# Kernel optimization log

Hardware: AMD Instinct MI355X
Metric: run time of the kernel (lower is better)

Reference implementation:

```python
import jax, jax.numpy as jnp
import numpy as np

KW, KH = 8, 8   # kernel_size = (kw, kh) per torch module indexing
SW, SH = 4, 4   # stride_size = (sw, sh)


def setup_inputs() -> dict:
    key = jax.random.key(0)
    x = jax.random.normal(key, (4, 128, 128, 128), dtype=jnp.float32)  # [B, C, H, W]
    return {"x": x}


def _local_autocorr(x, kh=KH, kw=KW, sh=SH, sw=SW):
    B, C, H, W = x.shape
    nh = (H - kh) // sh + 1
    nw = (W - kw) // sw + 1
    # Background is x zero-padded by (kh//2, (kh+1)//2 - 1) vertically and
    # (kw//2, (kw+1)//2 - 1) horizontally -> background patches are (2kh-1, 2kw-1).
    xp = jnp.pad(x, ((0, 0), (0, 0),
                     (kh // 2, (kh + 1) // 2 - 1),
                     (kw // 2, (kw + 1) // 2 - 1)))

    # For each shift (dy, dx) in [0,kh)x[0,kw):
    #   ret[b,iy,ix,c,dy,dx] = sum_{u,v} x[b,c,top+u,left+v] * xp[b,c,top+dy+u,left+dx+v]
    # i.e. elementwise product with the shifted map, then sum-pool with window (kh,kw), stride (sh,sw).
    def step(carry, s):
        dy = s // kw
        dx = s % kw
        shifted = jax.lax.dynamic_slice(xp, (0, 0, dy, dx), (B, C, H, W))
        prod = x * shifted
        pooled = jax.lax.reduce_window(prod, 0.0, jax.lax.add,
                                       (1, 1, kh, kw), (1, 1, sh, sw), 'VALID')
        return carry, pooled  # [B, C, nh, nw]

    _, stacked = jax.lax.scan(step, None, jnp.arange(kh * kw))
    # stacked: [kh*kw, B, C, nh, nw] with shift index s = dy*kw + dx
    out = stacked.reshape(kh, kw, B, C, nh, nw)
    out = jnp.transpose(out, (2, 4, 5, 3, 0, 1))  # [B, nh, nw, C, kh, kw]
    return out


def reference(x):
    return _local_autocorr(x)
```

## Files before the change

kernel.cpp:

```cpp
#include <hip/hip_runtime.h>


#define Bn 4
#define Cn 128
#define Hn 128
#define Wn 128
#define NH 31
#define NW 31
#define CB 16
#define PXT 4
#define PYT 4
#define TROWS 27
#define RST 28
#define CST (TROWS*RST)
#define F4C (TROWS*7)
#define PST 273

__global__ __launch_bounds__(256, 3)
void lac_kernel(const float* __restrict__ x, float* __restrict__ out) {
    __shared__ float sm[CB * CST];

    const int bid = blockIdx.x;
    const int ct = bid & 7;
    const int tx = (bid >> 3) & 7;
    const int ty = (bid >> 6) & 7;
    const int b  = bid >> 9;
    const int c0 = ct * CB;
    const int gy0 = ty * (PYT * 4) - 4;
    const int gx0 = tx * (PXT * 4) - 4;
    const int tid = threadIdx.x;

    for (int i = tid; i < CB * F4C; i += 256) {
        const int c   = i / F4C;
        const int rem = i - c * F4C;
        const int r   = rem / 7;
        const int q   = rem - r * 7;
        const int y   = gy0 + r;
        const int xc  = gx0 + q * 4;
        const float* src = x + (((size_t)(b * Cn + c0 + c) * Hn + y) * Wn + xc);
        float4 v;
        if (y >= 0 && y < Hn && xc >= 0 && xc + 3 < Wn) {
            v = *reinterpret_cast<const float4*>(src);
        } else if (y >= 0 && y < Hn) {
            v.x = (xc + 0 >= 0 && xc + 0 < Wn) ? src[0] : 0.0f;
            v.y = (xc + 1 >= 0 && xc + 1 < Wn) ? src[1] : 0.0f;
            v.z = (xc + 2 >= 0 && xc + 2 < Wn) ? src[2] : 0.0f;
            v.w = (xc + 3 >= 0 && xc + 3 < Wn) ? src[3] : 0.0f;
        } else {
            v = make_float4(0.0f, 0.0f, 0.0f, 0.0f);
        }
        reinterpret_cast<float4*>(sm)[i] = v;
    }
    __syncthreads();

    const int cs  = tid & 15;
    const int pos = tid >> 4;
    const int px  = pos & 3;
    const int py  = pos >> 2;
    const float* rg = &sm[cs * CST + (py * 4) * RST + px * 4];

    float acc[8][8];
#pragma unroll
    for (int i = 0; i < 8; ++i)
#pragma unroll
        for (int j = 0; j < 8; ++j) acc[i][j] = 0.0f;

#pragma unroll
    for (int r = 0; r < 15; ++r) {
        float rw[16];
        float4 q0 = *reinterpret_cast<const float4*>(&rg[r * RST + 0]);
        float4 q1 = *reinterpret_cast<const float4*>(&rg[r * RST + 4]);
        float4 q2 = *reinterpret_cast<const float4*>(&rg[r * RST + 8]);
        float4 q3 = *reinterpret_cast<const float4*>(&rg[r * RST + 12]);
        rw[0]  = q0.x; rw[1]  = q0.y; rw[2]  = q0.z; rw[3]  = q0.w;
        rw[4]  = q1.x; rw[5]  = q1.y; rw[6]  = q1.z; rw[7]  = q1.w;
        rw[8]  = q2.x; rw[9]  = q2.y; rw[10] = q2.z; rw[11] = q2.w;
        rw[12] = q3.x; rw[13] = q3.y; rw[14] = q3.z; rw[15] = q3.w;
#pragma unroll
        for (int u = 0; u < 8; ++u) {
            const int dy = r - u;
            if (dy >= 0 && dy < 8) {
                float4 b0 = *reinterpret_cast<const float4*>(&rg[(u + 4) * RST + 4]);
                float4 b1 = *reinterpret_cast<const float4*>(&rg[(u + 4) * RST + 8]);
                float bsr[8];
                bsr[0] = b0.x; bsr[1] = b0.y; bsr[2] = b0.z; bsr[3] = b0.w;
                bsr[4] = b1.x; bsr[5] = b1.y; bsr[6] = b1.z; bsr[7] = b1.w;
#pragma unroll
                for (int v = 0; v < 8; ++v) {
                    const float bv = bsr[v];
#pragma unroll
                    for (int dx = 0; dx < 8; ++dx)
                        acc[dy][dx] = fmaf(bv, rw[v + dx], acc[dy][dx]);
                }
            }
        }
    }

    float4* lds4 = reinterpret_cast<float4*>(sm);
#pragma unroll
    for (int rnd = 0; rnd < 2; ++rnd) {
        __syncthreads();
        if ((pos >> 3) == rnd) {
            const int p = pos & 7;
#pragma unroll
            for (int dy = 0; dy < 8; ++dy) {
                lds4[p * PST + cs * 17 + dy * 2 + 0] =
                    make_float4(acc[dy][0], acc[dy][1], acc[dy][2], acc[dy][3]);
                lds4[p * PST + cs * 17 + dy * 2 + 1] =
                    make_float4(acc[dy][4], acc[dy][5], acc[dy][6], acc[dy][7]);
            }
        }
        __syncthreads();
#pragma unroll
        for (int p = 0; p < 8; ++p) {
            const int pp  = rnd * 8 + p;
            const int ppx = pp & 3;
            const int ppy = pp >> 2;
            const int iy  = ty * PYT + ppy;
            const int ix  = tx * PXT + ppx;
            if (iy < NH && ix < NW) {
                float4* obase = reinterpret_cast<float4*>(
                    out + ((((size_t)b * NH + iy) * NW + ix) * Cn + c0) * 64);
                const int c   = tid >> 4;
                const int rem = tid & 15;
                obase[tid] = lds4[p * PST + c * 17 + rem];
            }
        }
    }
}

extern "C" void kernel_launch(void* const* d_in, const int* in_sizes, int n_in,
                              void* d_out, int out_size, void* d_ws, size_t ws_size,
                              hipStream_t stream) {
    const float* x = (const float*)d_in[0];
    float* out = (float*)d_out;
    lac_kernel<<<dim3(2048), dim3(256), 0, stream>>>(x, out);
}
```

Before: 94.35 us.

## Retile blocks to 8 channels by 8x4 positions and rework output staging

```diff
diff --git a/kernel.cpp b/kernel.cpp
--- a/kernel.cpp
+++ b/kernel.cpp
@@ -7,22 +7,24 @@
 #define Wn 128
 #define NH 31
 #define NW 31
-#define CB 16
-#define PXT 4
+#define CB 8
+#define PXT 8
 #define PYT 4
 #define TROWS 27
-#define RST 28
+#define RST 44
 #define CST (TROWS*RST)
-#define F4C (TROWS*7)
-#define PST 273
+#define F4C (TROWS*11)
+#define TPST 137
+#define TCST 17
 
-__global__ __launch_bounds__(256, 3)
+__global__ __launch_bounds__(256)
+__attribute__((amdgpu_waves_per_eu(4, 4)))
 void lac_kernel(const float* __restrict__ x, float* __restrict__ out) {
     __shared__ float sm[CB * CST];
 
     const int bid = blockIdx.x;
-    const int ct = bid & 7;
-    const int tx = (bid >> 3) & 7;
+    const int ct = bid & 15;
+    const int tx = (bid >> 4) & 3;
     const int ty = (bid >> 6) & 7;
     const int b  = bid >> 9;
     const int c0 = ct * CB;
@@ -33,8 +35,8 @@
     for (int i = tid; i < CB * F4C; i += 256) {
         const int c   = i / F4C;
         const int rem = i - c * F4C;
-        const int r   = rem / 7;
-        const int q   = rem - r * 7;
+        const int r   = rem / 11;
+        const int q   = rem - r * 11;
         const int y   = gy0 + r;
         const int xc  = gx0 + q * 4;
         const float* src = x + (((size_t)(b * Cn + c0 + c) * Hn + y) * Wn + xc);
@@ -53,10 +55,10 @@
     }
     __syncthreads();
 
-    const int cs  = tid & 15;
-    const int pos = tid >> 4;
-    const int px  = pos & 3;
-    const int py  = pos >> 2;
+    const int cs  = tid & 7;
+    const int pos = tid >> 3;
+    const int px  = pos & 7;
+    const int py  = pos >> 3;
     const float* rg = &sm[cs * CST + (py * 4) * RST + px * 4];
 
     float acc[8][8];
@@ -98,32 +100,31 @@
 
     float4* lds4 = reinterpret_cast<float4*>(sm);
 #pragma unroll
-    for (int rnd = 0; rnd < 2; ++rnd) {
+    for (int rnd = 0; rnd < 4; ++rnd) {
         __syncthreads();
-        if ((pos >> 3) == rnd) {
-            const int p = pos & 7;
+        if (py == rnd) {
+            const int p = px;
 #pragma unroll
             for (int dy = 0; dy < 8; ++dy) {
-                lds4[p * PST + cs * 17 + dy * 2 + 0] =
+                lds4[p * TPST + cs * TCST + dy * 2 + 0] =
                     make_float4(acc[dy][0], acc[dy][1], acc[dy][2], acc[dy][3]);
-                lds4[p * PST + cs * 17 + dy * 2 + 1] =
+                lds4[p * TPST + cs * TCST + dy * 2 + 1] =
                     make_float4(acc[dy][4], acc[dy][5], acc[dy][6], acc[dy][7]);
             }
         }
         __syncthreads();
+        const int iy = ty * PYT + rnd;
+        if (iy < NH) {
 #pragma unroll
-        for (int p = 0; p < 8; ++p) {
-            const int pp  = rnd * 8 + p;
-            const int ppx = pp & 3;
-            const int ppy = pp >> 2;
-            const int iy  = ty * PYT + ppy;
-            const int ix  = tx * PXT + ppx;
-            if (iy < NH && ix < NW) {
-                float4* obase = reinterpret_cast<float4*>(
-                    out + ((((size_t)b * NH + iy) * NW + ix) * Cn + c0) * 64);
-                const int c   = tid >> 4;
-                const int rem = tid & 15;
-                obase[tid] = lds4[p * PST + c * 17 + rem];
+            for (int sp = 0; sp < 4; ++sp) {
+                const int p  = sp * 2 + (tid >> 7);
+                const int ix = tx * PXT + p;
+                if (ix < NW) {
+                    const int j = tid & 127;
+                    float4* obase = reinterpret_cast<float4*>(
+                        out + ((((size_t)b * NH + iy) * NW + ix) * Cn + c0) * 64);
+                    obase[j] = lds4[p * TPST + (j >> 4) * TCST + (j & 15)];
+                }
             }
         }
     }
```

New measurement: 204.9 us. 2.17x slower.
